# Performance work log

Hardware: AMD Instinct MI355X
Metric: run time of the kernel (lower is better)

Reference implementation:

```python
import jax, jax.numpy as jnp
import numpy as np
from jax import lax

IC, OC, KS, HYP = 16, 16, 3, 128
BS, D = 4, 96

def setup_inputs() -> dict:
    key = jax.random.key(0)
    ks = jax.random.split(key, 6)
    x = jax.random.normal(ks[0], (BS, IC, D, D, D), dtype=jnp.float32)
    hyp_tensor = jax.random.normal(ks[1], (BS, HYP), dtype=jnp.float32)
    Wk = jax.random.normal(ks[2], (KS*KS*KS*IC*OC, HYP), dtype=jnp.float32) * 0.02
    bk = jax.random.normal(ks[3], (KS*KS*KS*IC*OC,), dtype=jnp.float32) * 0.02
    Wb = jax.random.normal(ks[4], (OC, HYP), dtype=jnp.float32) * 0.02
    bb = jax.random.normal(ks[5], (OC,), dtype=jnp.float32) * 0.02
    return {"x": x, "hyp_tensor": hyp_tensor, "Wk": Wk, "bk": bk, "Wb": Wb, "bb": bb}

def reference(x, hyp_tensor, Wk, bk, Wb, bb):
    bs = x.shape[0]
    # hypernetwork: per-sample kernels and biases (torch Linear: y = h @ W.T + b)
    kernel = (hyp_tensor @ Wk.T + bk).reshape(bs, OC, IC, KS, KS, KS)
    bias = hyp_tensor @ Wb.T + bb                      # [bs, OC]
    # per-sample conv == grouped conv with groups = bs
    xg = x.reshape(1, bs * IC, D, D, D)                # [1, bs*IC, D,H,W]
    kg = kernel.reshape(bs * OC, IC, KS, KS, KS)       # [bs*OC, IC, k,k,k]
    out = lax.conv_general_dilated(
        xg, kg,
        window_strides=(1, 1, 1),
        padding=[(1, 1)] * 3,
        feature_group_count=bs,
        dimension_numbers=("NCDHW", "OIDHW", "NCDHW"),
    )
    out = out.reshape(bs, OC, D, D, D) + bias[:, :, None, None, None]
    return out
```

## Files before the change

### kernel.cpp

```cpp
#include <hip/hip_runtime.h>

#define Dm 96
#define PL (Dm*Dm*Dm)
#define ICn 16
#define OCn 16
#define HYPn 128
#define BSn 4
#define NKK 14
#define FRAG_ELEMS (NKK*64*8)

typedef float   f32x4  __attribute__((ext_vector_type(4)));
typedef __bf16  bf16x8 __attribute__((ext_vector_type(8)));

__device__ __forceinline__ unsigned short f2bf(float f) {
    unsigned u = __builtin_bit_cast(unsigned, f);
    u = (u + 0x7FFFu + ((u >> 16) & 1u)) >> 16;
    return (unsigned short)u;
}

__global__ __launch_bounds__(256)
void hyper_frag_kernel(const float* __restrict__ hyp, const float* __restrict__ Wk,
                       const float* __restrict__ bk, unsigned short* __restrict__ kwf)
{
    int t = blockIdx.x * 256 + threadIdx.x;
    if (t >= BSn * FRAG_ELEMS) return;
    int j    = t & 7;
    int lane = (t >> 3) & 63;
    int rest = t >> 9;
    int kk   = rest % NKK;
    int b    = rest / NKK;
    int oc = lane & 15, hi = lane >> 4;
    int k  = kk * 32 + hi * 8 + j;
    int tap = k >> 4, ic = k & 15;
    float acc = 0.f;
    if (tap < 27) {
        int r = (oc * ICn + ic) * 27 + tap;
        const float4* w = (const float4*)(Wk + (long)r * HYPn);
        const float4* h = (const float4*)(hyp + (long)b * HYPn);
        acc = bk[r];
#pragma unroll
        for (int q = 0; q < HYPn / 4; ++q) {
            float4 a = h[q], c = w[q];
            acc += a.x * c.x + a.y * c.y + a.z * c.z + a.w * c.w;
        }
    }
    kwf[t] = f2bf(acc);
}

__global__ __launch_bounds__(64)
void hyper_bias_kernel(const float* __restrict__ hyp, const float* __restrict__ Wb,
                       const float* __restrict__ bb, float* __restrict__ bias)
{
    int t = threadIdx.x;
    int b = t >> 4, oc = t & 15;
    const float4* w = (const float4*)(Wb + (long)oc * HYPn);
    const float4* h = (const float4*)(hyp + (long)b * HYPn);
    float acc = bb[oc];
#pragma unroll
    for (int q = 0; q < HYPn / 4; ++q) {
        float4 a = h[q], c = w[q];
        acc += a.x * c.x + a.y * c.y + a.z * c.z + a.w * c.w;
    }
    bias[t] = acc;
}

#define ZT 4
#define YT 8
#define XT 16
#define ZL 6
#define YL 10
#define XL 18
#define SPN (ZL*YL*XL)
#define SSTR 48
#define LDSB (SPN*SSTR)

__device__ constexpr int tapoff(int t) {
    return (((t / 9) * YL + (t % 9) / 3) * XL + (t % 3)) * SSTR;
}

__global__ __launch_bounds__(256, 1)
void conv_mfma_kernel(const float* __restrict__ x, const unsigned short* __restrict__ kwf,
                      const float* __restrict__ bias, float* __restrict__ out)
{
    __shared__ __align__(16) char smem[LDSB];

    const int NXT = Dm / XT, NYT = Dm / YT, NZT = Dm / ZT;
    int raw = blockIdx.x;
    int bid = (raw & 7) * ((BSn * NXT * NYT * NZT) / 8) + (raw >> 3);

    int txi = bid % NXT; bid /= NXT;
    int tyi = bid % NYT; bid /= NYT;
    int tzi = bid % NZT;
    int b   = bid / NZT;
    int x0 = txi * XT, y0 = tyi * YT, z0 = tzi * ZT;

    int tid  = threadIdx.x;
    int lane = tid & 63;
    int wv   = tid >> 6;

    const float* xb = x + (long)b * ICn * PL;

    const unsigned short* kwb = kwf + (long)b * FRAG_ELEMS;
    bf16x8 afr[NKK];
#pragma unroll
    for (int kk = 0; kk < NKK; ++kk)
        afr[kk] = *(const bf16x8*)(kwb + (kk * 64 + lane) * 8);

    for (int t = tid; t < 2 * SPN; t += 256) {
        int ich = (t >= SPN) ? 1 : 0;
        int sp  = t - ich * SPN;
        int lx = sp % XL;
        int r  = sp / XL;
        int ly = r % YL;
        int lz = r / YL;
        int gz = z0 - 1 + lz, gy = y0 - 1 + ly, gx = x0 - 1 + lx;
        bf16x8 vv;
        if ((unsigned)gz < (unsigned)Dm && (unsigned)gy < (unsigned)Dm &&
            (unsigned)gx < (unsigned)Dm) {
            const float* g = xb + (long)(ich * 8) * PL + ((long)gz * Dm + gy) * Dm + gx;
#pragma unroll
            for (int q = 0; q < 8; ++q) vv[q] = (__bf16)g[(long)q * PL];
        } else {
#pragma unroll
            for (int q = 0; q < 8; ++q) vv[q] = (__bf16)0.f;
        }
        *(bf16x8*)(smem + sp * SSTR + ich * 16) = vv;
    }

    __syncthreads();

    int n    = lane & 15;
    int hi   = lane >> 4;
    int ich  = hi & 1;
    int tsel = hi >> 1;

    int addrk[NKK];
#pragma unroll
    for (int kk = 0; kk < NKK; ++kk) {
        int t0 = 2 * kk;
        int t1 = (2 * kk + 1 < 27) ? 2 * kk + 1 : 0;
        addrk[kk] = ((wv * YL) * XL + n) * SSTR + ich * 16 +
                    (tsel ? tapoff(t1) : tapoff(t0));
    }

    float4 bv = *(const float4*)(bias + b * OCn + hi * 4);

#pragma unroll 1
    for (int cp = 0; cp < YT / 2; ++cp) {
        f32x4 acc0 = {0.f, 0.f, 0.f, 0.f};
        f32x4 acc1 = {0.f, 0.f, 0.f, 0.f};
#pragma unroll
        for (int kk = 0; kk < NKK; ++kk) {
            bf16x8 f0 = *(const bf16x8*)(smem + addrk[kk]);
            bf16x8 f1 = *(const bf16x8*)(smem + addrk[kk] + XL * SSTR);
            acc0 = __builtin_amdgcn_mfma_f32_16x16x32_bf16(afr[kk], f0, acc0, 0, 0, 0);
            acc1 = __builtin_amdgcn_mfma_f32_16x16x32_bf16(afr[kk], f1, acc1, 0, 0, 0);
        }
        int zo = z0 + wv, yo = y0 + 2 * cp;
        long obase = ((((long)b * OCn + hi * 4) * Dm + zo) * Dm + yo) * Dm + x0 + n;
#pragma unroll
        for (int r = 0; r < 4; ++r) {
            out[obase + (long)r * PL]      = acc0[r] + ((const float*)&bv)[r];
            out[obase + (long)r * PL + Dm] = acc1[r] + ((const float*)&bv)[r];
        }
#pragma unroll
        for (int kk = 0; kk < NKK; ++kk) addrk[kk] += 2 * XL * SSTR;
    }
}

extern "C" void kernel_launch(void* const* d_in, const int* in_sizes, int n_in,
                              void* d_out, int out_size, void* d_ws, size_t ws_size,
                              hipStream_t stream)
{
    const float* x   = (const float*)d_in[0];
    const float* hyp = (const float*)d_in[1];
    const float* Wk  = (const float*)d_in[2];
    const float* bk  = (const float*)d_in[3];
    const float* Wb  = (const float*)d_in[4];
    const float* bb  = (const float*)d_in[5];
    float* out = (float*)d_out;

    unsigned short* kwf = (unsigned short*)d_ws;
    float* bias = (float*)((char*)d_ws + (size_t)BSn * FRAG_ELEMS * 2);

    hipLaunchKernelGGL(hyper_frag_kernel, dim3((BSn * FRAG_ELEMS) / 256), dim3(256), 0, stream,
                       hyp, Wk, bk, kwf);
    hipLaunchKernelGGL(hyper_bias_kernel, dim3(1), dim3(64), 0, stream,
                       hyp, Wb, bb, bias);

    const int nblk = BSn * (Dm / XT) * (Dm / YT) * (Dm / ZT);
    hipLaunchKernelGGL(conv_mfma_kernel, dim3(nblk), dim3(256), 0, stream,
                       x, kwf, bias, out);
}
```

Measured before the change: 185.7 us.

## Regroup conv taps by y-offset to reuse LDS fragments across output rows

The weight fragments are reorganized into 15 groups keyed by y tap offset (3 rows × 5 pairs of z/x taps), so each loaded LDS input row serves up to three output rows through a sliding-window accumulation. Each wave now computes 4 output rows with 6 row loads of 5 fragments instead of re-reading 14 fragments per row, which cuts LDS traffic. Blocks grow to 512 threads (8 waves) with launch bounds allowing 4 blocks per CU, raising occupancy. The cost is one extra padded MFMA group per row (15 vs 14) and more accumulator registers.

```diff
diff --git a/kernel.cpp b/kernel.cpp
--- a/kernel.cpp
+++ b/kernel.cpp
@@ -6,8 +6,8 @@
 #define OCn 16
 #define HYPn 128
 #define BSn 4
-#define NKK 14
-#define FRAG_ELEMS (NKK*64*8)
+#define NG 15
+#define FRAG_ELEMS (NG*64*8)
 
 typedef float   f32x4  __attribute__((ext_vector_type(4)));
 typedef __bf16  bf16x8 __attribute__((ext_vector_type(8)));
@@ -27,21 +27,24 @@
     int j    = t & 7;
     int lane = (t >> 3) & 63;
     int rest = t >> 9;
-    int kk   = rest % NKK;
-    int b    = rest / NKK;
+    int grp  = rest % NG;
+    int b    = rest / NG;
     int oc = lane & 15, hi = lane >> 4;
-    int k  = kk * 32 + hi * 8 + j;
-    int tap = k >> 4, ic = k & 15;
+    int ty = grp / 5, g = grp % 5;
+    int cl = hi >> 1;
+    int ic = (hi & 1) * 8 + j;
+    int c  = 2 * g + cl;
     float acc = 0.f;
-    if (tap < 27) {
-        int r = (oc * ICn + ic) * 27 + tap;
+    if (c < 9) {
+        int tz = c / 3, tx = c % 3;
+        int r = (oc * ICn + ic) * 27 + (tz * 9 + ty * 3 + tx);
         const float4* w = (const float4*)(Wk + (long)r * HYPn);
         const float4* h = (const float4*)(hyp + (long)b * HYPn);
         acc = bk[r];
 #pragma unroll
         for (int q = 0; q < HYPn / 4; ++q) {
-            float4 a = h[q], c = w[q];
-            acc += a.x * c.x + a.y * c.y + a.z * c.z + a.w * c.w;
+            float4 a = h[q], cc = w[q];
+            acc += a.x * cc.x + a.y * cc.y + a.z * cc.z + a.w * cc.w;
         }
     }
     kwf[t] = f2bf(acc);
@@ -74,11 +77,11 @@
 #define SSTR 48
 #define LDSB (SPN*SSTR)
 
-__device__ constexpr int tapoff(int t) {
-    return (((t / 9) * YL + (t % 9) / 3) * XL + (t % 3)) * SSTR;
-}
-
-__global__ __launch_bounds__(256, 1)
+__device__ constexpr int coff(int c) {
+    return ((c / 3) * YL * XL + (c % 3)) * SSTR;
+}
+
+__global__ __launch_bounds__(512, 4)
 void conv_mfma_kernel(const float* __restrict__ x, const unsigned short* __restrict__ kwf,
                       const float* __restrict__ bias, float* __restrict__ out)
 {
@@ -96,17 +99,19 @@
 
     int tid  = threadIdx.x;
     int lane = tid & 63;
-    int wv   = tid >> 6;
+    int wave = tid >> 6;
+    int wz   = wave & 3;
+    int wh   = wave >> 2;
 
     const float* xb = x + (long)b * ICn * PL;
 
     const unsigned short* kwb = kwf + (long)b * FRAG_ELEMS;
-    bf16x8 afr[NKK];
-#pragma unroll
-    for (int kk = 0; kk < NKK; ++kk)
-        afr[kk] = *(const bf16x8*)(kwb + (kk * 64 + lane) * 8);
-
-    for (int t = tid; t < 2 * SPN; t += 256) {
+    bf16x8 afr[NG];
+#pragma unroll
+    for (int grp = 0; grp < NG; ++grp)
+        afr[grp] = *(const bf16x8*)(kwb + (grp * 64 + lane) * 8);
+
+    for (int t = tid; t < 2 * SPN; t += 512) {
         int ich = (t >= SPN) ? 1 : 0;
         int sp  = t - ich * SPN;
         int lx = sp % XL;
@@ -129,42 +134,50 @@
 
     __syncthreads();
 
-    int n    = lane & 15;
-    int hi   = lane >> 4;
-    int ich  = hi & 1;
-    int tsel = hi >> 1;
-
-    int addrk[NKK];
-#pragma unroll
-    for (int kk = 0; kk < NKK; ++kk) {
-        int t0 = 2 * kk;
-        int t1 = (2 * kk + 1 < 27) ? 2 * kk + 1 : 0;
-        addrk[kk] = ((wv * YL) * XL + n) * SSTR + ich * 16 +
-                    (tsel ? tapoff(t1) : tapoff(t0));
+    int n   = lane & 15;
+    int hi  = lane >> 4;
+    int cl  = hi >> 1;
+    int ich = hi & 1;
+
+    int addr_g[5];
+#pragma unroll
+    for (int g = 0; g < 5; ++g) {
+        int c = 2 * g + cl;
+        if (c > 8) c = 8;
+        addr_g[g] = ((wz * YL + 4 * wh) * XL + n) * SSTR + ich * 16 + coff(c);
+    }
+
+    f32x4 acc[4];
+#pragma unroll
+    for (int yy = 0; yy < 4; ++yy) acc[yy] = (f32x4){0.f, 0.f, 0.f, 0.f};
+
+#pragma unroll
+    for (int p = 0; p < 6; ++p) {
+        bf16x8 F[5];
+#pragma unroll
+        for (int g = 0; g < 5; ++g)
+            F[g] = *(const bf16x8*)(smem + addr_g[g] + p * (XL * SSTR));
+#pragma unroll
+        for (int ty = 0; ty < 3; ++ty) {
+            int yy = p - ty;
+            if (yy >= 0 && yy < 4) {
+#pragma unroll
+                for (int g = 0; g < 5; ++g)
+                    acc[yy] = __builtin_amdgcn_mfma_f32_16x16x32_bf16(
+                        afr[ty * 5 + g], F[g], acc[yy], 0, 0, 0);
+            }
+        }
     }
 
     float4 bv = *(const float4*)(bias + b * OCn + hi * 4);
-
-#pragma unroll 1
-    for (int cp = 0; cp < YT / 2; ++cp) {
-        f32x4 acc0 = {0.f, 0.f, 0.f, 0.f};
-        f32x4 acc1 = {0.f, 0.f, 0.f, 0.f};
-#pragma unroll
-        for (int kk = 0; kk < NKK; ++kk) {
-            bf16x8 f0 = *(const bf16x8*)(smem + addrk[kk]);
-            bf16x8 f1 = *(const bf16x8*)(smem + addrk[kk] + XL * SSTR);
-            acc0 = __builtin_amdgcn_mfma_f32_16x16x32_bf16(afr[kk], f0, acc0, 0, 0, 0);
-            acc1 = __builtin_amdgcn_mfma_f32_16x16x32_bf16(afr[kk], f1, acc1, 0, 0, 0);
-        }
-        int zo = z0 + wv, yo = y0 + 2 * cp;
+    int zo = z0 + wz;
+#pragma unroll
+    for (int yy = 0; yy < 4; ++yy) {
+        int yo = y0 + 4 * wh + yy;
         long obase = ((((long)b * OCn + hi * 4) * Dm + zo) * Dm + yo) * Dm + x0 + n;
 #pragma unroll
-        for (int r = 0; r < 4; ++r) {
-            out[obase + (long)r * PL]      = acc0[r] + ((const float*)&bv)[r];
-            out[obase + (long)r * PL + Dm] = acc1[r] + ((const float*)&bv)[r];
-        }
-#pragma unroll
-        for (int kk = 0; kk < NKK; ++kk) addrk[kk] += 2 * XL * SSTR;
+        for (int r = 0; r < 4; ++r)
+            out[obase + (long)r * PL] = acc[yy][r] + ((const float*)&bv)[r];
     }
 }
 
@@ -189,6 +202,6 @@
                        hyp, Wb, bb, bias);
 
     const int nblk = BSn * (Dm / XT) * (Dm / YT) * (Dm / ZT);
-    hipLaunchKernelGGL(conv_mfma_kernel, dim3(nblk), dim3(256), 0, stream,
+    hipLaunchKernelGGL(conv_mfma_kernel, dim3(nblk), dim3(512), 0, stream,
                        x, kwf, bias, out);
 }
```

Result: slower. 195.2 us (+5.1%).
